# Kernel optimization log

Hardware: AMD Instinct MI355X
Metric: run time of the kernel (lower is better)

The kernel has to match this reference:

```python
import jax, jax.numpy as jnp
import numpy as np

S = 7
STEP = 1.0 / 7
LAMBDA_COORD = 5.0
LAMBDA_NOOBJ = 0.5
NUM_CLASS = 20
D = 10 + NUM_CLASS  # 30 channels per cell
BATCH = 8192


def setup_inputs() -> dict:
    key = jax.random.key(0)
    k1, k2, k3 = jax.random.split(key, 3)
    pred = jax.random.uniform(k1, (BATCH, S, S, D), dtype=jnp.float32)
    target = jax.random.uniform(k2, (BATCH, S, S, D), dtype=jnp.float32)
    obj = jax.random.uniform(k3, (BATCH, S, S)) < 0.2
    target = target.at[..., 4].set(jnp.where(obj, 1.0, 0.0))
    return {"pred": pred, "target": target}


def _convert(box, ii, jj):
    # conver_box: cell-relative (x,y,w,h) -> image-space top-left corner + size
    x, y, w, h = box[..., 0], box[..., 1], box[..., 2], box[..., 3]
    x = (x + jj) * STEP
    y = (y + ii) * STEP
    a = jnp.maximum(x - w / 2, 0.0)
    b = jnp.maximum(y - h / 2, 0.0)
    return a, b, w, h


def _iou(box1, box2, ii, jj):
    x1, y1, w1, h1 = _convert(box1, ii, jj)
    x2, y2, w2, h2 = _convert(box2, ii, jj)
    iw = w1 + w2 - (jnp.maximum(x1 + w1, x2 + w2) - jnp.minimum(x1, x2))
    ih = h1 + h2 - (jnp.maximum(y1 + h1, y2 + h2) - jnp.minimum(y1, y2))
    valid = (iw > 0) & (ih > 0)
    inter = jnp.where(valid, iw * ih, 0.0)
    union = w1 * h1 + w2 * h2 - inter
    return jnp.where(valid, inter / jnp.where(valid, union, 1.0), 0.0)


def reference(pred, target):
    B = pred.shape[0]
    dt = pred.dtype
    ii = jnp.arange(S, dtype=dt)[None, :, None]  # grid row index (dim 1)
    jj = jnp.arange(S, dtype=dt)[None, None, :]  # grid col index (dim 2)

    obj = target[..., 4] > 0
    noobj = target[..., 4] == 0

    tbox = target[..., 0:4]
    # .item() in the torch code detaches the IoU -> stop_gradient
    iou1 = jax.lax.stop_gradient(_iou(tbox, pred[..., 0:4], ii, jj))
    iou2 = jax.lax.stop_gradient(_iou(tbox, pred[..., 5:9], ii, jj))

    choose1 = iou1 > iou2
    # after responsibility assignment, rows with tc conf == 0 are dropped
    m1 = (obj & choose1 & (iou1 != 0)).astype(dt)   # box-1 responsible
    m2 = (obj & (~choose1) & (iou2 != 0)).astype(dt)  # box-2 responsible

    obj_loss = jnp.sum(m1 * (iou1 - pred[..., 4]) ** 2) + \
               jnp.sum(m2 * (iou2 - pred[..., 9]) ** 2)

    xy_loss = jnp.sum(m1[..., None] * (target[..., 0:2] - pred[..., 0:2]) ** 2) + \
              jnp.sum(m2[..., None] * (target[..., 5:7] - pred[..., 5:7]) ** 2)

    wh_loss = jnp.sum(m1[..., None] * (jnp.sqrt(target[..., 2:4]) - jnp.sqrt(pred[..., 2:4])) ** 2) + \
              jnp.sum(m2[..., None] * (jnp.sqrt(target[..., 7:9]) - jnp.sqrt(pred[..., 7:9])) ** 2)

    # faithful to pred[:, :10][noobj_mask].view(-1, 5)[:, 4]: the 30-channel
    # noobj rows are reshaped to (-1, 5), so conf channels hit 4,9,14,19,24,29
    conf_idx = jnp.array([4, 9, 14, 19, 24, 29])
    mn = noobj.astype(dt)
    noobj_loss = jnp.sum(mn[..., None] * (target[..., conf_idx] - pred[..., conf_idx]) ** 2)

    mo = obj.astype(dt)
    class_loss = jnp.sum(mo[..., None] * (pred[..., 10:] - target[..., 10:]) ** 2)

    conf_loss = (obj_loss + LAMBDA_NOOBJ * noobj_loss) / B
    reg_loss = (LAMBDA_COORD * xy_loss + LAMBDA_COORD * wh_loss) / B
    cls_loss = class_loss / B
    return jnp.stack([conf_loss, reg_loss, cls_loss])
```

## Files before the change

kernel.cpp:

```cpp
#include <hip/hip_runtime.h>

#define NCELLS (8192 * 7 * 7)
#define BLOCK 256
#define NSLOT 256

__device__ __forceinline__ float sq(float x) { return x * x; }

__device__ __forceinline__ float iou_fn(const float* t, const float* p, float fi, float fj) {
    const float STEP = 1.0f / 7.0f;
    float w1 = t[2], h1 = t[3];
    float x1 = (t[0] + fj) * STEP, y1 = (t[1] + fi) * STEP;
    float a1 = fmaxf(x1 - w1 * 0.5f, 0.0f);
    float b1 = fmaxf(y1 - h1 * 0.5f, 0.0f);
    float w2 = p[2], h2 = p[3];
    float x2 = (p[0] + fj) * STEP, y2 = (p[1] + fi) * STEP;
    float a2 = fmaxf(x2 - w2 * 0.5f, 0.0f);
    float b2 = fmaxf(y2 - h2 * 0.5f, 0.0f);
    float iw = w1 + w2 - (fmaxf(a1 + w1, a2 + w2) - fminf(a1, a2));
    float ih = h1 + h2 - (fmaxf(b1 + h1, b2 + h2) - fminf(b1, b2));
    bool valid = (iw > 0.0f) && (ih > 0.0f);
    float inter = valid ? iw * ih : 0.0f;
    float uni = w1 * h1 + w2 * h2 - inter;
    return valid ? inter / uni : 0.0f;
}

__global__ __launch_bounds__(BLOCK) void yolo_part_kernel(
        const float* __restrict__ pred, const float* __restrict__ target,
        float* __restrict__ partials) {
    const float invB = 1.0f / 8192.0f;
    int c = blockIdx.x * BLOCK + threadIdx.x;

    unsigned cell = (unsigned)c % 49u;
    float fi = (float)(cell / 7u);
    float fj = (float)(cell % 7u);

    const float* p = pred + (size_t)c * 30;
    const float* t = target + (size_t)c * 30;

    float pl[30], tl[30];
#pragma unroll
    for (int k = 0; k < 15; ++k) {
        float2 pv = ((const float2*)p)[k];
        float2 tv = ((const float2*)t)[k];
        pl[2 * k] = pv.x; pl[2 * k + 1] = pv.y;
        tl[2 * k] = tv.x; tl[2 * k + 1] = tv.y;
    }

    bool obj = tl[4] > 0.0f;

    float iou1 = iou_fn(tl, pl, fi, fj);
    float iou2 = iou_fn(tl, pl + 5, fi, fj);
    bool choose1 = iou1 > iou2;
    float m1 = (obj && choose1 && (iou1 != 0.0f)) ? 1.0f : 0.0f;
    float m2 = (obj && !choose1 && (iou2 != 0.0f)) ? 1.0f : 0.0f;

    float obj_loss = m1 * sq(iou1 - pl[4]) + m2 * sq(iou2 - pl[9]);

    float xy = m1 * (sq(tl[0] - pl[0]) + sq(tl[1] - pl[1]))
             + m2 * (sq(tl[5] - pl[5]) + sq(tl[6] - pl[6]));

    float wh = m1 * (sq(sqrtf(tl[2]) - sqrtf(pl[2])) + sq(sqrtf(tl[3]) - sqrtf(pl[3])))
             + m2 * (sq(sqrtf(tl[7]) - sqrtf(pl[7])) + sq(sqrtf(tl[8]) - sqrtf(pl[8])));

    float noobj = 0.0f;
#pragma unroll
    for (int k = 0; k < 6; ++k) {
        int ci = 4 + 5 * k;
        noobj += sq(tl[ci] - pl[ci]);
    }
    if (obj) noobj = 0.0f;

    float clsum = 0.0f;
#pragma unroll
    for (int k = 10; k < 30; ++k) clsum += sq(pl[k] - tl[k]);
    if (!obj) clsum = 0.0f;

    float conf = (obj_loss + 0.5f * noobj) * invB;
    float reg  = 5.0f * (xy + wh) * invB;
    float cls  = clsum * invB;

#pragma unroll
    for (int off = 32; off > 0; off >>= 1) {
        conf += __shfl_down(conf, off, 64);
        reg  += __shfl_down(reg,  off, 64);
        cls  += __shfl_down(cls,  off, 64);
    }

    __shared__ float s[3][4];
    int lane = threadIdx.x & 63;
    int wave = threadIdx.x >> 6;
    if (lane == 0) { s[0][wave] = conf; s[1][wave] = reg; s[2][wave] = cls; }
    __syncthreads();
    if (threadIdx.x == 0) {
        float* slot = partials + (size_t)(blockIdx.x & (NSLOT - 1)) * 4;
        atomicAdd(&slot[0], s[0][0] + s[0][1] + s[0][2] + s[0][3]);
        atomicAdd(&slot[1], s[1][0] + s[1][1] + s[1][2] + s[1][3]);
        atomicAdd(&slot[2], s[2][0] + s[2][1] + s[2][2] + s[2][3]);
    }
}

__global__ __launch_bounds__(BLOCK) void yolo_final_kernel(
        const float4* __restrict__ partials, float* __restrict__ out) {
    int tid = threadIdx.x;
    float4 v = partials[tid];
    float a = v.x, b = v.y, d = v.z;
#pragma unroll
    for (int off = 32; off > 0; off >>= 1) {
        a += __shfl_down(a, off, 64);
        b += __shfl_down(b, off, 64);
        d += __shfl_down(d, off, 64);
    }
    __shared__ float s[3][4];
    int lane = tid & 63;
    int wave = tid >> 6;
    if (lane == 0) { s[0][wave] = a; s[1][wave] = b; s[2][wave] = d; }
    __syncthreads();
    if (tid == 0) {
        out[0] = s[0][0] + s[0][1] + s[0][2] + s[0][3];
        out[1] = s[1][0] + s[1][1] + s[1][2] + s[1][3];
        out[2] = s[2][0] + s[2][1] + s[2][2] + s[2][3];
    }
}

extern "C" void kernel_launch(void* const* d_in, const int* in_sizes, int n_in,
                              void* d_out, int out_size, void* d_ws, size_t ws_size,
                              hipStream_t stream) {
    const float* pred   = (const float*)d_in[0];
    const float* target = (const float*)d_in[1];
    float* out = (float*)d_out;
    float* partials = (float*)d_ws;

    hipMemsetAsync(d_ws, 0, NSLOT * 4 * sizeof(float), stream);

    int grid = NCELLS / BLOCK;
    yolo_part_kernel<<<grid, BLOCK, 0, stream>>>(pred, target, partials);
    yolo_final_kernel<<<1, BLOCK, 0, stream>>>((const float4*)partials, out);
}
```

Baseline: 114.0 us.

## Use grid-stride persistent blocks and fuse final reduction via direct atomics

Replaces the one-thread-per-cell launch with a fixed grid of 512 blocks that grid-stride over cells and accumulate locally. It also removes the second reduction kernel, with each block atomically adding its scaled sums straight into the three outputs. This cuts block count, atomic traffic and one launch. The cost is fewer resident waves to hide memory latency, and 512 blocks contending on the same three atomic addresses.

```diff
diff --git a/kernel.cpp b/kernel.cpp
--- a/kernel.cpp
+++ b/kernel.cpp
@@ -2,7 +2,7 @@
 
 #define NCELLS (8192 * 7 * 7)
 #define BLOCK 256
-#define NSLOT 256
+#define GRID 512
 
 __device__ __forceinline__ float sq(float x) { return x * x; }
 
@@ -24,60 +24,61 @@
     return valid ? inter / uni : 0.0f;
 }
 
-__global__ __launch_bounds__(BLOCK) void yolo_part_kernel(
+__global__ __launch_bounds__(BLOCK) void yolo_fused_kernel(
         const float* __restrict__ pred, const float* __restrict__ target,
-        float* __restrict__ partials) {
-    const float invB = 1.0f / 8192.0f;
-    int c = blockIdx.x * BLOCK + threadIdx.x;
+        float* __restrict__ out) {
+    float conf = 0.0f, reg = 0.0f, cls = 0.0f;
 
-    unsigned cell = (unsigned)c % 49u;
-    float fi = (float)(cell / 7u);
-    float fj = (float)(cell % 7u);
+    for (int c = blockIdx.x * BLOCK + threadIdx.x; c < NCELLS; c += GRID * BLOCK) {
+        unsigned cell = (unsigned)c % 49u;
+        float fi = (float)(cell / 7u);
+        float fj = (float)(cell % 7u);
 
-    const float* p = pred + (size_t)c * 30;
-    const float* t = target + (size_t)c * 30;
+        const float* p = pred + (size_t)c * 30;
+        const float* t = target + (size_t)c * 30;
 
-    float pl[30], tl[30];
+        float pl[30], tl[30];
 #pragma unroll
-    for (int k = 0; k < 15; ++k) {
-        float2 pv = ((const float2*)p)[k];
-        float2 tv = ((const float2*)t)[k];
-        pl[2 * k] = pv.x; pl[2 * k + 1] = pv.y;
-        tl[2 * k] = tv.x; tl[2 * k + 1] = tv.y;
+        for (int k = 0; k < 15; ++k) {
+            float2 pv = ((const float2*)p)[k];
+            float2 tv = ((const float2*)t)[k];
+            pl[2 * k] = pv.x; pl[2 * k + 1] = pv.y;
+            tl[2 * k] = tv.x; tl[2 * k + 1] = tv.y;
+        }
+
+        bool obj = tl[4] > 0.0f;
+
+        float iou1 = iou_fn(tl, pl, fi, fj);
+        float iou2 = iou_fn(tl, pl + 5, fi, fj);
+        bool choose1 = iou1 > iou2;
+        float m1 = (obj && choose1 && (iou1 != 0.0f)) ? 1.0f : 0.0f;
+        float m2 = (obj && !choose1 && (iou2 != 0.0f)) ? 1.0f : 0.0f;
+
+        float obj_loss = m1 * sq(iou1 - pl[4]) + m2 * sq(iou2 - pl[9]);
+
+        float xy = m1 * (sq(tl[0] - pl[0]) + sq(tl[1] - pl[1]))
+                 + m2 * (sq(tl[5] - pl[5]) + sq(tl[6] - pl[6]));
+
+        float wh = m1 * (sq(sqrtf(tl[2]) - sqrtf(pl[2])) + sq(sqrtf(tl[3]) - sqrtf(pl[3])))
+                 + m2 * (sq(sqrtf(tl[7]) - sqrtf(pl[7])) + sq(sqrtf(tl[8]) - sqrtf(pl[8])));
+
+        float noobj = 0.0f;
+#pragma unroll
+        for (int k = 0; k < 6; ++k) {
+            int ci = 4 + 5 * k;
+            noobj += sq(tl[ci] - pl[ci]);
+        }
+        if (obj) noobj = 0.0f;
+
+        float clsum = 0.0f;
+#pragma unroll
+        for (int k = 10; k < 30; ++k) clsum += sq(pl[k] - tl[k]);
+        if (!obj) clsum = 0.0f;
+
+        conf += obj_loss + 0.5f * noobj;
+        reg  += xy + wh;
+        cls  += clsum;
     }
-
-    bool obj = tl[4] > 0.0f;
-
-    float iou1 = iou_fn(tl, pl, fi, fj);
-    float iou2 = iou_fn(tl, pl + 5, fi, fj);
-    bool choose1 = iou1 > iou2;
-    float m1 = (obj && choose1 && (iou1 != 0.0f)) ? 1.0f : 0.0f;
-    float m2 = (obj && !choose1 && (iou2 != 0.0f)) ? 1.0f : 0.0f;
-
-    float obj_loss = m1 * sq(iou1 - pl[4]) + m2 * sq(iou2 - pl[9]);
-
-    float xy = m1 * (sq(tl[0] - pl[0]) + sq(tl[1] - pl[1]))
-             + m2 * (sq(tl[5] - pl[5]) + sq(tl[6] - pl[6]));
-
-    float wh = m1 * (sq(sqrtf(tl[2]) - sqrtf(pl[2])) + sq(sqrtf(tl[3]) - sqrtf(pl[3])))
-             + m2 * (sq(sqrtf(tl[7]) - sqrtf(pl[7])) + sq(sqrtf(tl[8]) - sqrtf(pl[8])));
-
-    float noobj = 0.0f;
-#pragma unroll
-    for (int k = 0; k < 6; ++k) {
-        int ci = 4 + 5 * k;
-        noobj += sq(tl[ci] - pl[ci]);
-    }
-    if (obj) noobj = 0.0f;
-
-    float clsum = 0.0f;
-#pragma unroll
-    for (int k = 10; k < 30; ++k) clsum += sq(pl[k] - tl[k]);
-    if (!obj) clsum = 0.0f;
-
-    float conf = (obj_loss + 0.5f * noobj) * invB;
-    float reg  = 5.0f * (xy + wh) * invB;
-    float cls  = clsum * invB;
 
 #pragma unroll
     for (int off = 32; off > 0; off >>= 1) {
@@ -92,33 +93,10 @@
     if (lane == 0) { s[0][wave] = conf; s[1][wave] = reg; s[2][wave] = cls; }
     __syncthreads();
     if (threadIdx.x == 0) {
-        float* slot = partials + (size_t)(blockIdx.x & (NSLOT - 1)) * 4;
-        atomicAdd(&slot[0], s[0][0] + s[0][1] + s[0][2] + s[0][3]);
-        atomicAdd(&slot[1], s[1][0] + s[1][1] + s[1][2] + s[1][3]);
-        atomicAdd(&slot[2], s[2][0] + s[2][1] + s[2][2] + s[2][3]);
-    }
-}
-
-__global__ __launch_bounds__(BLOCK) void yolo_final_kernel(
-        const float4* __restrict__ partials, float* __restrict__ out) {
-    int tid = threadIdx.x;
-    float4 v = partials[tid];
-    float a = v.x, b = v.y, d = v.z;
-#pragma unroll
-    for (int off = 32; off > 0; off >>= 1) {
-        a += __shfl_down(a, off, 64);
-        b += __shfl_down(b, off, 64);
-        d += __shfl_down(d, off, 64);
-    }
-    __shared__ float s[3][4];
-    int lane = tid & 63;
-    int wave = tid >> 6;
-    if (lane == 0) { s[0][wave] = a; s[1][wave] = b; s[2][wave] = d; }
-    __syncthreads();
-    if (tid == 0) {
-        out[0] = s[0][0] + s[0][1] + s[0][2] + s[0][3];
-        out[1] = s[1][0] + s[1][1] + s[1][2] + s[1][3];
-        out[2] = s[2][0] + s[2][1] + s[2][2] + s[2][3];
+        const float invB = 1.0f / 8192.0f;
+        atomicAdd(&out[0], (s[0][0] + s[0][1] + s[0][2] + s[0][3]) * invB);
+        atomicAdd(&out[1], (s[1][0] + s[1][1] + s[1][2] + s[1][3]) * (5.0f * invB));
+        atomicAdd(&out[2], (s[2][0] + s[2][1] + s[2][2] + s[2][3]) * invB);
     }
 }
 
@@ -128,11 +106,8 @@
     const float* pred   = (const float*)d_in[0];
     const float* target = (const float*)d_in[1];
     float* out = (float*)d_out;
-    float* partials = (float*)d_ws;
 
-    hipMemsetAsync(d_ws, 0, NSLOT * 4 * sizeof(float), stream);
+    hipMemsetAsync(d_out, 0, 3 * sizeof(float), stream);
 
-    int grid = NCELLS / BLOCK;
-    yolo_part_kernel<<<grid, BLOCK, 0, stream>>>(pred, target, partials);
-    yolo_final_kernel<<<1, BLOCK, 0, stream>>>((const float4*)partials, out);
+    yolo_fused_kernel<<<GRID, BLOCK, 0, stream>>>(pred, target, out);
 }
```

Result: slower. 124.5 us (+9.2%).

## Stage cell data through LDS with coalesced float4 loads and drop atomics

Applied to the files above, without the earlier changes.

Each block now loads its 128 cells of pred and target into shared memory with fully coalesced float4 loads, then each thread reads its own 30-channel record from LDS. Before, each thread made strided float2 global loads. Per-block partials are written directly to a float4 array instead of atomically added into 256 slots. This removes the memset and the atomic contention. The final kernel loops over all 3136 partials, so it does more serial work, and the LDS reads at a stride of 30 floats may cause bank conflicts.

```diff
diff --git a/kernel.cpp b/kernel.cpp
--- a/kernel.cpp
+++ b/kernel.cpp
@@ -1,8 +1,9 @@
 #include <hip/hip_runtime.h>
 
 #define NCELLS (8192 * 7 * 7)
-#define BLOCK 256
-#define NSLOT 256
+#define BLOCK 128
+#define CPB 128
+#define NBLOCKS (NCELLS / CPB)
 
 __device__ __forceinline__ float sq(float x) { return x * x; }
 
@@ -26,25 +27,29 @@
 
 __global__ __launch_bounds__(BLOCK) void yolo_part_kernel(
         const float* __restrict__ pred, const float* __restrict__ target,
-        float* __restrict__ partials) {
-    const float invB = 1.0f / 8192.0f;
-    int c = blockIdx.x * BLOCK + threadIdx.x;
+        float4* __restrict__ partials) {
+    __shared__ float s[2 * CPB * 30];
+    const int tid = threadIdx.x;
 
+    const size_t blockBase = (size_t)blockIdx.x * (CPB * 30);
+    const float4* gp = (const float4*)(pred + blockBase);
+    const float4* gt = (const float4*)(target + blockBase);
+    float4* ls = (float4*)s;
+#pragma unroll
+    for (int r = 0; r < 15; ++r) {
+        int i = r * BLOCK + tid;
+        const float4* base = (i < 960) ? gp : (gt - 960);
+        ls[i] = base[i];
+    }
+    __syncthreads();
+
+    int c = blockIdx.x * CPB + tid;
     unsigned cell = (unsigned)c % 49u;
     float fi = (float)(cell / 7u);
     float fj = (float)(cell % 7u);
 
-    const float* p = pred + (size_t)c * 30;
-    const float* t = target + (size_t)c * 30;
-
-    float pl[30], tl[30];
-#pragma unroll
-    for (int k = 0; k < 15; ++k) {
-        float2 pv = ((const float2*)p)[k];
-        float2 tv = ((const float2*)t)[k];
-        pl[2 * k] = pv.x; pl[2 * k + 1] = pv.y;
-        tl[2 * k] = tv.x; tl[2 * k + 1] = tv.y;
-    }
+    const float* pl = s + tid * 30;
+    const float* tl = s + CPB * 30 + tid * 30;
 
     bool obj = tl[4] > 0.0f;
 
@@ -75,9 +80,9 @@
     for (int k = 10; k < 30; ++k) clsum += sq(pl[k] - tl[k]);
     if (!obj) clsum = 0.0f;
 
-    float conf = (obj_loss + 0.5f * noobj) * invB;
-    float reg  = 5.0f * (xy + wh) * invB;
-    float cls  = clsum * invB;
+    float conf = obj_loss + 0.5f * noobj;
+    float reg  = xy + wh;
+    float cls  = clsum;
 
 #pragma unroll
     for (int off = 32; off > 0; off >>= 1) {
@@ -86,24 +91,29 @@
         cls  += __shfl_down(cls,  off, 64);
     }
 
-    __shared__ float s[3][4];
-    int lane = threadIdx.x & 63;
-    int wave = threadIdx.x >> 6;
-    if (lane == 0) { s[0][wave] = conf; s[1][wave] = reg; s[2][wave] = cls; }
+    __shared__ float sr[3][2];
+    int lane = tid & 63;
+    int wave = tid >> 6;
+    if (lane == 0) { sr[0][wave] = conf; sr[1][wave] = reg; sr[2][wave] = cls; }
     __syncthreads();
-    if (threadIdx.x == 0) {
-        float* slot = partials + (size_t)(blockIdx.x & (NSLOT - 1)) * 4;
-        atomicAdd(&slot[0], s[0][0] + s[0][1] + s[0][2] + s[0][3]);
-        atomicAdd(&slot[1], s[1][0] + s[1][1] + s[1][2] + s[1][3]);
-        atomicAdd(&slot[2], s[2][0] + s[2][1] + s[2][2] + s[2][3]);
+    if (tid == 0) {
+        const float invB = 1.0f / 8192.0f;
+        partials[blockIdx.x] = make_float4(
+            (sr[0][0] + sr[0][1]) * invB,
+            (sr[1][0] + sr[1][1]) * (5.0f * invB),
+            (sr[2][0] + sr[2][1]) * invB,
+            0.0f);
     }
 }
 
-__global__ __launch_bounds__(BLOCK) void yolo_final_kernel(
+__global__ __launch_bounds__(256) void yolo_final_kernel(
         const float4* __restrict__ partials, float* __restrict__ out) {
     int tid = threadIdx.x;
-    float4 v = partials[tid];
-    float a = v.x, b = v.y, d = v.z;
+    float a = 0.0f, b = 0.0f, d = 0.0f;
+    for (int i = tid; i < NBLOCKS; i += 256) {
+        float4 v = partials[i];
+        a += v.x; b += v.y; d += v.z;
+    }
 #pragma unroll
     for (int off = 32; off > 0; off >>= 1) {
         a += __shfl_down(a, off, 64);
@@ -128,11 +138,7 @@
     const float* pred   = (const float*)d_in[0];
     const float* target = (const float*)d_in[1];
     float* out = (float*)d_out;
-    float* partials = (float*)d_ws;
-
-    hipMemsetAsync(d_ws, 0, NSLOT * 4 * sizeof(float), stream);
-
-    int grid = NCELLS / BLOCK;
-    yolo_part_kernel<<<grid, BLOCK, 0, stream>>>(pred, target, partials);
-    yolo_final_kernel<<<1, BLOCK, 0, stream>>>((const float4*)partials, out);
+    float4* partials = (float4*)d_ws;
+    yolo_part_kernel<<<NBLOCKS, BLOCK, 0, stream>>>(pred, target, partials);
+    yolo_final_kernel<<<1, 256, 0, stream>>>(partials, out);
 }
```

New measurement: 113.5 us. Within noise of the previous version (-0.4%).
